# Kernel tuning notes

Measured on AMD Instinct MI355X. Metric: run time of the kernel, lower is better.

The kernel has to match this reference:

```python
import jax, jax.numpy as jnp
import numpy as np

B, S, E = 4, 2048, 1024
H = E // 2  # per-head dim (2 heads)


def setup_inputs() -> dict:
    key = jax.random.key(0)
    ks = jax.random.split(key, 10)
    w = 0.02
    return {
        "input": jax.random.normal(ks[0], (B, S, E), dtype=jnp.float32),
        "Wq": jax.random.normal(ks[1], (2, H, H), dtype=jnp.float32) * w,
        "bq": jax.random.normal(ks[2], (2, H), dtype=jnp.float32) * w,
        "Wk": jax.random.normal(ks[3], (2, H, H), dtype=jnp.float32) * w,
        "bk": jax.random.normal(ks[4], (2, H), dtype=jnp.float32) * w,
        "Wv": jax.random.normal(ks[5], (2, H, H), dtype=jnp.float32) * w,
        "bv": jax.random.normal(ks[6], (2, H), dtype=jnp.float32) * w,
        "Wf": jax.random.normal(ks[7], (E, E), dtype=jnp.float32) * w,
        "bf": jax.random.normal(ks[8], (E,), dtype=jnp.float32) * w,
        "masked": 1,
    }


def reference(input, Wq, bq, Wk, bk, Wv, bv, Wf, bf, masked):
    b, s, e = input.shape
    h = e // 2
    # contiguous split into 2 heads: [b, s, 2, h]
    xh = input.reshape(b, s, 2, h)
    # per-head Linear: y = x @ W.T + b  (W is [out, in])
    q = jnp.einsum("bsnh,noh->bsno", xh, Wq) + bq
    k = jnp.einsum("bsnh,noh->bsno", xh, Wk) + bk
    v = jnp.einsum("bsnh,noh->bsno", xh, Wv) + bv
    # scores: [b, n, s, t]
    scores = jnp.einsum("bsno,btno->bnst", q, k) / jnp.sqrt(jnp.float32(h))
    if masked:
        causal = jnp.tril(jnp.ones((s, s), dtype=bool))
        scores = jnp.where(causal, scores, jnp.float32(-jnp.inf))
    probs = jax.nn.softmax(scores, axis=-1)
    out = jnp.einsum("bnst,btnh->bsnh", probs, v).reshape(b, s, e)
    return jnp.einsum("bse,oe->bso", out, Wf) + bf
```

## Files before the change

kernel.cpp:

```cpp
#include <hip/hip_runtime.h>
#include <hip/hip_bf16.h>

#define BB 4
#define SS 2048
#define EE 1024
#define HH 512

typedef __attribute__((ext_vector_type(8))) short short8;
typedef __attribute__((ext_vector_type(4))) float f32x4;
typedef __attribute__((ext_vector_type(16))) float f32x16;
typedef __attribute__((ext_vector_type(4))) unsigned short us4;

static __device__ __forceinline__ unsigned short f2bf(float x){
  unsigned u = __float_as_uint(x);
  u += 0x7fffu + ((u >> 16) & 1u);
  return (unsigned short)(u >> 16);
}

static __device__ __forceinline__ unsigned cvtpk(float lo, float hi){
  unsigned d;
  asm("v_cvt_pk_bf16_f32 %0, %1, %2" : "=v"(d) : "v"(lo), "v"(hi));
  return d;
}

static __device__ __forceinline__ void gload16(const void* g, void* l){
  __builtin_amdgcn_global_load_lds((const __attribute__((address_space(1))) void*)g,
                                   (__attribute__((address_space(3))) void*)l, 16, 0, 0);
}

__global__ void k_cvt_all(const float* __restrict__ x,  const float* __restrict__ wq,
                          const float* __restrict__ wk, const float* __restrict__ wv,
                          const float* __restrict__ wf,
                          unsigned short* __restrict__ xb,  unsigned short* __restrict__ wqb,
                          unsigned short* __restrict__ wkb, unsigned short* __restrict__ wvb,
                          unsigned short* __restrict__ wfb){
  const int N0 = 1048576;
  const int N1 = N0 + 65536;
  const int N2 = N1 + 65536;
  const int N3 = N2 + 65536;
  const int N4 = N3 + 131072;
  int idx = blockIdx.x * blockDim.x + threadIdx.x;
  int stride = gridDim.x * blockDim.x;
  for (int i = idx; i < N4; i += stride){
    const float* src; unsigned short* dst; int j;
    if (i < N0){ src = x;  dst = xb;  j = i; }
    else if (i < N1){ src = wq; dst = wqb; j = i - N0; }
    else if (i < N2){ src = wk; dst = wkb; j = i - N1; }
    else if (i < N3){ src = wv; dst = wvb; j = i - N2; }
    else            { src = wf; dst = wfb; j = i - N3; }
    const float4* p = (const float4*)src + (long)j * 2;
    float4 a = p[0], b = p[1];
    union { unsigned short u[8]; uint4 v; } r;
    r.u[0]=f2bf(a.x); r.u[1]=f2bf(a.y); r.u[2]=f2bf(a.z); r.u[3]=f2bf(a.w);
    r.u[4]=f2bf(b.x); r.u[5]=f2bf(b.y); r.u[6]=f2bf(b.z); r.u[7]=f2bf(b.w);
    ((uint4*)dst)[j] = r.v;
  }
}

#define GBK 32

template<int OUTMODE>
static __device__ __forceinline__ void gemm_tile(
    const unsigned short* __restrict__ A, int lda,
    const unsigned short* __restrict__ Bw, int ldb,
    void* __restrict__ Cc, int ldc,
    const float* __restrict__ bias, int K, int row0, int col0, float oscale)
{
  __shared__ unsigned short As[2][128 * GBK];
  __shared__ unsigned short Bs[2][128 * GBK];
  const int tid = threadIdx.x, lane = tid & 63, w = tid >> 6;
  const int wm = w >> 1, wn = w & 1;
  const int fr = lane & 15, g = lane >> 4;

  f32x4 acc[4][4];
  #pragma unroll
  for (int i = 0; i < 4; i++)
    #pragma unroll
    for (int j = 0; j < 4; j++){ acc[i][j][0]=0.f; acc[i][j][1]=0.f; acc[i][j][2]=0.f; acc[i][j][3]=0.f; }

  const unsigned short* gAsrc[2]; const unsigned short* gBsrc[2];
  unsigned ldsOff[2];
  #pragma unroll
  for (int i = 0; i < 2; i++){
    int slot = w*128 + i*64 + lane;
    int row = slot >> 2, ch = slot & 3;
    int sc_ = ch ^ ((row >> 1) & 3);
    gAsrc[i] = A  + (long)(row0 + row) * lda + sc_ * 8;
    gBsrc[i] = Bw + (long)(col0 + row) * ldb + sc_ * 8;
    ldsOff[i] = (unsigned)((w*128 + i*64) * 8);
  }

  unsigned aoff[4], boff[4];
  #pragma unroll
  for (int mi = 0; mi < 4; mi++){
    int row = wm*64 + mi*16 + fr;
    aoff[mi] = row * GBK + ((g ^ ((row >> 1) & 3)) * 8);
  }
  #pragma unroll
  for (int ni = 0; ni < 4; ni++){
    int row = wn*64 + ni*16 + fr;
    boff[ni] = row * GBK + ((g ^ ((row >> 1) & 3)) * 8);
  }

  const int KT = K / GBK;
  #pragma unroll
  for (int i = 0; i < 2; i++) gload16(gAsrc[i], &As[0][ldsOff[i]]);
  #pragma unroll
  for (int i = 0; i < 2; i++) gload16(gBsrc[i], &Bs[0][ldsOff[i]]);
  __syncthreads();

  for (int kt = 0; kt < KT; ++kt){
    const int cur = kt & 1;
    if (kt + 1 < KT){
      #pragma unroll
      for (int i = 0; i < 2; i++) gload16(gAsrc[i] + (kt+1)*GBK, &As[cur^1][ldsOff[i]]);
      #pragma unroll
      for (int i = 0; i < 2; i++) gload16(gBsrc[i] + (kt+1)*GBK, &Bs[cur^1][ldsOff[i]]);
    }
    short8 av[4], bv[4];
    #pragma unroll
    for (int mi = 0; mi < 4; mi++) av[mi] = *(const short8*)&As[cur][aoff[mi]];
    #pragma unroll
    for (int ni = 0; ni < 4; ni++) bv[ni] = *(const short8*)&Bs[cur][boff[ni]];
    #pragma unroll
    for (int mi = 0; mi < 4; mi++)
      #pragma unroll
      for (int ni = 0; ni < 4; ni++)
        acc[mi][ni] = __builtin_amdgcn_mfma_f32_16x16x32_bf16(av[mi], bv[ni], acc[mi][ni], 0, 0, 0);
    __syncthreads();
  }

  if constexpr (OUTMODE == 2){
    __shared__ unsigned short Ct[128][136];
    #pragma unroll
    for (int mi = 0; mi < 4; mi++){
      #pragma unroll
      for (int ni = 0; ni < 4; ni++){
        int rowb = wm*64 + mi*16 + g*4;
        int col  = wn*64 + ni*16 + fr;
        float bb = bias[col0 + col];
        us4 pk;
        #pragma unroll
        for (int r = 0; r < 4; r++) pk[r] = f2bf((acc[mi][ni][r] + bb) * oscale);
        *(us4*)&Ct[col][rowb] = pk;
      }
    }
    __syncthreads();
    #pragma unroll
    for (int it = 0; it < 8; it++){
      int idx2 = it * 256 + tid;
      int o = idx2 >> 4, sch = idx2 & 15;
      uint4 v = *(const uint4*)&Ct[o][sch * 8];
      *(uint4*)&((unsigned short*)Cc)[(long)(col0 + o) * ldc + row0 + sch * 8] = v;
    }
  } else {
    #pragma unroll
    for (int mi = 0; mi < 4; mi++){
      #pragma unroll
      for (int ni = 0; ni < 4; ni++){
        int row = row0 + wm*64 + mi*16 + g*4;
        int col = col0 + wn*64 + ni*16 + fr;
        float bb = bias[col];
        #pragma unroll
        for (int r = 0; r < 4; r++){
          float v = (acc[mi][ni][r] + bb) * oscale;
          if (OUTMODE == 1) ((unsigned short*)Cc)[(long)(row + r) * ldc + col] = f2bf(v);
          else              ((float*)Cc)[(long)(row + r) * ldc + col] = v;
        }
      }
    }
  }
}

__global__ __launch_bounds__(256, 2) void k_qkv(
    const unsigned short* __restrict__ xb,
    const unsigned short* __restrict__ wq, const unsigned short* __restrict__ wk,
    const float* __restrict__ bq, const float* __restrict__ bk,
    unsigned short* __restrict__ Q, unsigned short* __restrict__ K)
{
  int z = blockIdx.z; int which = z >> 3; int bn = z & 7; int b = bn >> 1, n = bn & 1;
  const unsigned short* W; const float* bias; unsigned short* out;
  float os = 1.f;
  if (which == 0){ W = wq; bias = bq; out = Q; os = 0.044194173824159216f; }
  else { W = wk; bias = bk; out = K; }
  W += n * HH * HH; bias += n * HH; out += (long)bn * SS * HH;
  const unsigned short* Ap = xb + (long)b * SS * EE + n * HH;
  gemm_tile<1>(Ap, EE, W, HH, out, HH, bias, HH, blockIdx.x * 128, blockIdx.y * 128, os);
}

__global__ __launch_bounds__(256, 2) void k_qkv_v(
    const unsigned short* __restrict__ xb, const unsigned short* __restrict__ wv,
    const float* __restrict__ bv, unsigned short* __restrict__ Vt)
{
  int bn = blockIdx.z; int b = bn >> 1, n = bn & 1;
  const unsigned short* W = wv + n * HH * HH;
  const float* bias = bv + n * HH;
  unsigned short* out = Vt + (long)bn * SS * HH;
  const unsigned short* Ap = xb + (long)b * SS * EE + n * HH;
  gemm_tile<2>(Ap, EE, W, HH, out, SS, bias, HH, blockIdx.x * 128, blockIdx.y * 128, 1.f);
}

__global__ __launch_bounds__(256, 2) void k_outproj(
    const unsigned short* __restrict__ O, const unsigned short* __restrict__ wf,
    const float* __restrict__ bfb, float* __restrict__ out)
{
  gemm_tile<0>(O, EE, wf, EE, out, EE, bfb, EE, blockIdx.x * 128, blockIdx.y * 128, 1.f);
}

#define QB 128
#define TB 32

__global__ __launch_bounds__(512, 1) void k_flash10(
    const unsigned short* __restrict__ Qg, const unsigned short* __restrict__ Kg,
    const unsigned short* __restrict__ Vtg,
    unsigned short* __restrict__ Opart, float* __restrict__ mlg,
    const int* __restrict__ maskedp)
{
  __shared__ unsigned short Ks[2][TB * HH];
  __shared__ unsigned short Vs[HH * TB];
  __shared__ float2 Sx[4][2][8][64];

  const int bid = blockIdx.x;
  const int bn = bid & 7;
  const int u = bid >> 3;
  const int masked = *maskedp;
  int qi, c;
  if (masked){
    qi = -1; c = 0;
    int cnt = 0;
    #pragma unroll 1
    for (int q = 0; q < 16; q++){
      int nch = (4*q + 25) / 22;
      if (qi < 0 && u >= cnt && u < cnt + nch){ qi = q; c = u - cnt; }
      cnt += nch;
    }
    if (qi < 0) return;
  } else { qi = u >> 1; c = u & 1; }
  const int n  = masked ? 4*qi + 4 : 64;
  const int CH = masked ? 22 : 32;
  const int t0 = c * CH;
  const int t1 = min(n, t0 + CH);

  const long base = (long)bn * SS * HH;
  const unsigned short* Qp = Qg + base;
  const unsigned short* Kp = Kg + base;
  const unsigned short* Vp = Vtg + base;

  const int tid = threadIdx.x, lane = tid & 63, w = tid >> 6;
  const int ln = lane & 31, hi = lane >> 5;
  const int rg = w & 3, dh = w >> 2;
  const int q0 = qi * QB;
  const int myq = q0 + rg * 32 + ln;

  short8 Qr[16];
  {
    const unsigned short* qrow = Qp + (long)myq * HH + dh * 256 + hi * 8;
    #pragma unroll
    for (int ks = 0; ks < 16; ks++) Qr[ks] = *(const short8*)(qrow + ks * 16);
  }

  f32x16 oa[8];
  #pragma unroll
  for (int i = 0; i < 8; i++)
    #pragma unroll
    for (int r = 0; r < 16; r++) oa[i][r] = 0.f;
  float m_r = -1e30f, l_r = 0.f;

  auto stageK = [&](int buf, int t){
    if (w < 4){
      #pragma unroll
      for (int i = 0; i < 8; i++){
        const int sbase = w * 512 + i * 64;
        const int slot = sbase + lane;
        int row = slot >> 6, ch = slot & 63;
        int sc_ = ch ^ (row & 7);
        gload16(Kp + (long)(t * TB + row) * HH + sc_ * 8, &Ks[buf][sbase * 8]);
      }
    }
  };
  auto stageV = [&](int t){
    if (w >= 4){
      #pragma unroll
      for (int i = 0; i < 8; i++){
        const int sbase = (w - 4) * 512 + i * 64;
        const int slot = sbase + lane;
        int row = slot >> 2, ch = slot & 3;
        int sc_ = ch ^ ((row >> 1) & 3);
        gload16(Vp + (long)row * SS + t * TB + sc_ * 8, &Vs[sbase * 8]);
      }
    }
  };

  stageK(0, t0);
  stageV(t0);
  __syncthreads();

  for (int t = t0; t < t1; ++t){
    const int cur = (t - t0) & 1;
    if (t > t0)     stageV(t);
    if (t + 1 < t1) stageK(cur ^ 1, t + 1);

    f32x16 sa;
    #pragma unroll
    for (int r = 0; r < 16; r++) sa[r] = 0.f;
    #pragma unroll
    for (int ks = 0; ks < 16; ks++){
      int ch = (dh * 32 + ks * 2 + hi) ^ (ln & 7);
      short8 kf = *(const short8*)&Ks[cur][ln * HH + ch * 8];
      sa = __builtin_amdgcn_mfma_f32_32x32x16_bf16(kf, Qr[ks], sa, 0, 0, 0);
    }

    #pragma unroll
    for (int i = 0; i < 8; i++)
      Sx[rg][dh][i][lane] = make_float2(sa[2*i], sa[2*i+1]);

    __syncthreads();

    float p[16];
    #pragma unroll
    for (int i = 0; i < 8; i++){
      float2 o = Sx[rg][dh ^ 1][i][lane];
      p[2*i]   = sa[2*i]   + o.x;
      p[2*i+1] = sa[2*i+1] + o.y;
    }

    if (masked && (t * TB + TB - 1 > myq)){
      #pragma unroll
      for (int r = 0; r < 16; r++){
        int tl = (r & 3) + 8 * (r >> 2) + 4 * hi;
        if (t * TB + tl > myq) p[r] = -1e30f;
      }
    }

    float mx = p[0];
    #pragma unroll
    for (int r = 1; r < 16; r++) mx = fmaxf(mx, p[r]);
    mx = fmaxf(mx, __shfl_xor(mx, 32, 64));
    if (__any(mx > m_r + 8.f)){
      float mn = fmaxf(m_r, mx);
      float alpha = __expf(m_r - mn);
      m_r = mn; l_r *= alpha;
      #pragma unroll
      for (int r = 0; r < 16; r++){
        float al = __shfl(alpha, (r & 3) + 8 * (r >> 2) + 4 * hi, 64);
        #pragma unroll
        for (int i = 0; i < 8; i++) oa[i][r] *= al;
      }
    }
    float ps = 0.f;
    #pragma unroll
    for (int r = 0; r < 16; r++){ float pe = __expf(p[r] - m_r); p[r] = pe; ps += pe; }
    ps += __shfl_xor(ps, 32, 64);
    l_r += ps;

    unsigned W[8], R[8];
    #pragma unroll
    for (int i = 0; i < 8; i++) W[i] = cvtpk(p[2*i], p[2*i+1]);
    #pragma unroll
    for (int i = 0; i < 8; i++) R[i] = __shfl_xor(W[i], 32, 64);
    union { unsigned u[4]; short8 s; } fa0, fa1;
    fa0.u[0] = hi ? R[2] : W[0];  fa0.u[1] = hi ? R[3] : W[1];
    fa0.u[2] = hi ? W[2] : R[0];  fa0.u[3] = hi ? W[3] : R[1];
    fa1.u[0] = hi ? R[6] : W[4];  fa1.u[1] = hi ? R[7] : W[5];
    fa1.u[2] = hi ? W[6] : R[4];  fa1.u[3] = hi ? W[7] : R[5];

    #pragma unroll
    for (int cf = 0; cf < 8; cf++){
      int h = dh * 256 + cf * 32 + ln;
      int sw = (h >> 1) & 3;
      short8 v0 = *(const short8*)&Vs[h * TB + ((hi     ^ sw) * 8)];
      oa[cf] = __builtin_amdgcn_mfma_f32_32x32x16_bf16(fa0.s, v0, oa[cf], 0, 0, 0);
      short8 v1 = *(const short8*)&Vs[h * TB + (((2+hi) ^ sw) * 8)];
      oa[cf] = __builtin_amdgcn_mfma_f32_32x32x16_bf16(fa1.s, v1, oa[cf], 0, 0, 0);
    }

    __syncthreads();
  }

  const long slot = (long)(bn * 16 + qi) * 3 + c;
  unsigned short* dst = Opart + slot * (QB * HH);
  #pragma unroll
  for (int cf = 0; cf < 8; cf++){
    int col = dh * 256 + cf * 32 + ln;
    #pragma unroll
    for (int r = 0; r < 16; r++){
      int row = rg * 32 + (r & 3) + 8 * (r >> 2) + 4 * hi;
      dst[row * HH + col] = f2bf(oa[cf][r]);
    }
  }
  if (w < 4 && hi == 0){
    mlg[slot * 256 + rg * 32 + ln]       = m_r;
    mlg[slot * 256 + 128 + rg * 32 + ln] = l_r;
  }
}

__global__ __launch_bounds__(256) void k_combine(
    const unsigned short* __restrict__ Opart, const float* __restrict__ mlg,
    unsigned short* __restrict__ O, const int* __restrict__ maskedp)
{
  __shared__ float wl[128][3];
  const int gq = blockIdx.x;
  const int bn = gq & 7, qi = gq >> 3;
  const int b = bn >> 1, n = bn & 1;
  const int NC = (*maskedp) ? (4*qi + 25) / 22 : 2;
  const long slotbase = (long)(bn * 16 + qi) * 3;
  const int tid = threadIdx.x;

  if (tid < 128){
    float mc[3], lc[3];
    float M = -1e30f;
    for (int c = 0; c < NC; c++){
      mc[c] = mlg[(slotbase + c) * 256 + tid];
      lc[c] = mlg[(slotbase + c) * 256 + 128 + tid];
      M = fmaxf(M, mc[c]);
    }
    float L = 0.f;
    for (int c = 0; c < NC; c++){
      float wc = __expf(mc[c] - M);
      mc[c] = wc;
      L += lc[c] * wc;
    }
    float inv = 1.f / L;
    #pragma unroll
    for (int c = 0; c < 3; c++) wl[tid][c] = (c < NC) ? mc[c] * inv : 0.f;
  }
  __syncthreads();

  for (int it = 0; it < 32; it++){
    int idx = it * 256 + tid;
    int row = idx >> 6, cv = idx & 63;
    float acc[8] = {0.f,0.f,0.f,0.f,0.f,0.f,0.f,0.f};
    for (int c = 0; c < NC; c++){
      float wc = wl[row][c];
      short8 v = *(const short8*)&Opart[(slotbase + c) * (QB * HH) + row * HH + cv * 8];
      #pragma unroll
      for (int j = 0; j < 8; j++){
        float f = __uint_as_float((unsigned)(unsigned short)v[j] << 16);
        acc[j] += f * wc;
      }
    }
    union { unsigned short u[8]; uint4 q; } rr;
    #pragma unroll
    for (int j = 0; j < 8; j++) rr.u[j] = f2bf(acc[j]);
    long dstoff = ((long)b * SS + qi * QB + row) * EE + n * HH + cv * 8;
    *(uint4*)&O[dstoff] = rr.q;
  }
}

extern "C" void kernel_launch(void* const* d_in, const int* in_sizes, int n_in,
                              void* d_out, int out_size, void* d_ws, size_t ws_size,
                              hipStream_t stream)
{
  const float* x   = (const float*)d_in[0];
  const float* Wq  = (const float*)d_in[1];
  const float* bq  = (const float*)d_in[2];
  const float* Wk  = (const float*)d_in[3];
  const float* bk  = (const float*)d_in[4];
  const float* Wv  = (const float*)d_in[5];
  const float* bv  = (const float*)d_in[6];
  const float* Wf  = (const float*)d_in[7];
  const float* bf_ = (const float*)d_in[8];
  const int* masked = (const int*)d_in[9];

  char* p = (char*)d_ws;
  const long TEN = (long)BB * SS * EE * 2;
  unsigned short* xb  = (unsigned short*)p; p += TEN;
  unsigned short* Qb  = (unsigned short*)p; p += TEN;
  unsigned short* Kb  = (unsigned short*)p; p += TEN;
  unsigned short* Vt  = (unsigned short*)p; p += TEN;
  unsigned short* Ob  = (unsigned short*)p; p += TEN;
  unsigned short* wqb = (unsigned short*)p; p += 2L * HH * HH * 2;
  unsigned short* wkb = (unsigned short*)p; p += 2L * HH * HH * 2;
  unsigned short* wvb = (unsigned short*)p; p += 2L * HH * HH * 2;
  unsigned short* wfb = (unsigned short*)p; p += (long)EE * EE * 2;
  unsigned short* Opart = (unsigned short*)p; p += 384L * QB * HH * 2;
  float* mlg = (float*)p; p += 384L * 256 * 4;

  k_cvt_all<<<dim3(2048), 256, 0, stream>>>(x, Wq, Wk, Wv, Wf, xb, wqb, wkb, wvb, wfb);
  k_qkv    <<<dim3(SS / 128, HH / 128, 16), 256, 0, stream>>>(xb, wqb, wkb, bq, bk, Qb, Kb);
  k_qkv_v  <<<dim3(SS / 128, HH / 128, 8),  256, 0, stream>>>(xb, wvb, bv, Vt);
  k_flash10<<<dim3(256), 512, 0, stream>>>(Qb, Kb, Vt, Opart, mlg, masked);
  k_combine<<<dim3(128), 256, 0, stream>>>(Opart, mlg, Ob, masked);
  k_outproj<<<dim3((BB * SS) / 128, EE / 128, 1), 256, 0, stream>>>(Ob, wfb, bf_, (float*)d_out);
}
```

Measured before the change: 231.7 us.

## Fuse split-KV combine into output projection GEMM A-tile loading

Removes the separate combine kernel and the intermediate O buffer. The output-projection GEMM now reads the partial attention outputs and their (m, l) statistics directly, merges the partials with softmax weights while building each A tile in shared memory, and writes bf16 A tiles itself instead of using async loads. This saves one launch and a round trip of the O tensor through memory. In exchange, the combine work is repeated for every column block (8 times) and the A path becomes register-staged rather than async, adding ALU and load pressure inside the GEMM main loop.

Result: slower. 240.2 us (+3.7%).

```diff
diff --git a/kernel.cpp b/kernel.cpp
--- a/kernel.cpp
+++ b/kernel.cpp
@@ -164,8 +164,7 @@
         #pragma unroll
         for (int r = 0; r < 4; r++){
           float v = (acc[mi][ni][r] + bb) * oscale;
-          if (OUTMODE == 1) ((unsigned short*)Cc)[(long)(row + r) * ldc + col] = f2bf(v);
-          else              ((float*)Cc)[(long)(row + r) * ldc + col] = v;
+          ((unsigned short*)Cc)[(long)(row + r) * ldc + col] = f2bf(v);
         }
       }
     }
@@ -200,17 +199,165 @@
   gemm_tile<2>(Ap, EE, W, HH, out, SS, bias, HH, blockIdx.x * 128, blockIdx.y * 128, 1.f);
 }
 
-__global__ __launch_bounds__(256, 2) void k_outproj(
-    const unsigned short* __restrict__ O, const unsigned short* __restrict__ wf,
-    const float* __restrict__ bfb, float* __restrict__ out)
+__global__ __launch_bounds__(256, 2) void k_outproj_f(
+    const unsigned short* __restrict__ Opart, const float* __restrict__ mlg,
+    const unsigned short* __restrict__ wf, const float* __restrict__ bfb,
+    float* __restrict__ out, const int* __restrict__ maskedp)
 {
-  gemm_tile<0>(O, EE, wf, EE, out, EE, bfb, EE, blockIdx.x * 128, blockIdx.y * 128, 1.f);
+  __shared__ unsigned short As[2][128 * GBK];
+  __shared__ unsigned short Bs[2][128 * GBK];
+  __shared__ float wl2[2][128][3];
+
+  const int tid = threadIdx.x, lane = tid & 63, w = tid >> 6;
+  const int wm = w >> 1, wn = w & 1;
+  const int fr = lane & 15, g = lane >> 4;
+  const int row0 = blockIdx.x * 128, col0 = blockIdx.y * 128;
+  const int b = row0 >> 11, qi = (row0 & 2047) >> 7;
+  const int masked = *maskedp;
+  const int NC = masked ? (4*qi + 25) / 22 : 2;
+  const long sbn[2] = { ((long)(b*2+0)*16 + qi) * 3, ((long)(b*2+1)*16 + qi) * 3 };
+
+  {
+    int nn = tid >> 7, r = tid & 127;
+    long sb = sbn[nn];
+    float mc[3], lc[3], M = -1e30f;
+    for (int c = 0; c < NC; c++){
+      mc[c] = mlg[(sb + c) * 256 + r];
+      lc[c] = mlg[(sb + c) * 256 + 128 + r];
+      M = fmaxf(M, mc[c]);
+    }
+    float L = 0.f;
+    for (int c = 0; c < NC; c++){ float e = __expf(mc[c] - M); mc[c] = e; L += lc[c] * e; }
+    float inv = 1.f / L;
+    #pragma unroll
+    for (int c = 0; c < 3; c++) wl2[nn][r][c] = (c < NC) ? mc[c] * inv : 0.f;
+  }
+  __syncthreads();
+
+  int rowv[2], scv[2], slotv[2];
+  float wlr0[2][3], wlr1[2][3];
+  #pragma unroll
+  for (int i = 0; i < 2; i++){
+    int slot = w*128 + i*64 + lane;
+    slotv[i] = slot;
+    rowv[i] = slot >> 2;
+    scv[i] = (slot & 3) ^ ((rowv[i] >> 1) & 3);
+    #pragma unroll
+    for (int c = 0; c < 3; c++){
+      wlr0[i][c] = wl2[0][rowv[i]][c];
+      wlr1[i][c] = wl2[1][rowv[i]][c];
+    }
+  }
+
+  const unsigned short* gBsrc[2];
+  unsigned ldsOffB[2];
+  #pragma unroll
+  for (int i = 0; i < 2; i++){
+    int slot = w*128 + i*64 + lane;
+    int row = slot >> 2, ch = slot & 3;
+    int sc_ = ch ^ ((row >> 1) & 3);
+    gBsrc[i] = wf + (long)(col0 + row) * EE + sc_ * 8;
+    ldsOffB[i] = (unsigned)((w*128 + i*64) * 8);
+  }
+
+  unsigned aoff[4], boff[4];
+  #pragma unroll
+  for (int mi = 0; mi < 4; mi++){
+    int row = wm*64 + mi*16 + fr;
+    aoff[mi] = row * GBK + ((g ^ ((row >> 1) & 3)) * 8);
+  }
+  #pragma unroll
+  for (int ni = 0; ni < 4; ni++){
+    int row = wn*64 + ni*16 + fr;
+    boff[ni] = row * GBK + ((g ^ ((row >> 1) & 3)) * 8);
+  }
+
+  f32x4 acc[4][4];
+  #pragma unroll
+  for (int i = 0; i < 4; i++)
+    #pragma unroll
+    for (int j = 0; j < 4; j++){ acc[i][j][0]=0.f; acc[i][j][1]=0.f; acc[i][j][2]=0.f; acc[i][j][3]=0.f; }
+
+  uint4 va[2][3];
+  auto loadA = [&](int kt){
+    const int nn = kt >> 4;
+    const long sb = nn ? sbn[1] : sbn[0];
+    #pragma unroll
+    for (int i = 0; i < 2; i++){
+      long base = sb * 65536L + (long)rowv[i] * HH + (kt & 15) * 32 + scv[i] * 8;
+      #pragma unroll
+      for (int c = 0; c < 3; c++)
+        if (c < NC) va[i][c] = *(const uint4*)&Opart[base + c * 65536L];
+    }
+  };
+  auto writeA = [&](int buf, int kt){
+    const int nn = kt >> 4;
+    #pragma unroll
+    for (int i = 0; i < 2; i++){
+      float a8[8] = {0.f,0.f,0.f,0.f,0.f,0.f,0.f,0.f};
+      #pragma unroll
+      for (int c = 0; c < 3; c++){
+        if (c < NC){
+          float wc = nn ? wlr1[i][c] : wlr0[i][c];
+          const unsigned short* pu = (const unsigned short*)&va[i][c];
+          #pragma unroll
+          for (int j = 0; j < 8; j++)
+            a8[j] += __uint_as_float((unsigned)pu[j] << 16) * wc;
+        }
+      }
+      union { unsigned short u[8]; uint4 q; } pk;
+      #pragma unroll
+      for (int j = 0; j < 8; j++) pk.u[j] = f2bf(a8[j]);
+      *(uint4*)&As[buf][slotv[i] * 8] = pk.q;
+    }
+  };
+
+  const int KT = EE / GBK;
+  loadA(0);
+  writeA(0, 0);
+  #pragma unroll
+  for (int i = 0; i < 2; i++) gload16(gBsrc[i], &Bs[0][ldsOffB[i]]);
+  __syncthreads();
+
+  for (int kt = 0; kt < KT; ++kt){
+    const int cur = kt & 1;
+    if (kt + 1 < KT){
+      loadA(kt + 1);
+      #pragma unroll
+      for (int i = 0; i < 2; i++) gload16(gBsrc[i] + (kt+1)*GBK, &Bs[cur^1][ldsOffB[i]]);
+    }
+    short8 av[4], bv[4];
+    #pragma unroll
+    for (int mi = 0; mi < 4; mi++) av[mi] = *(const short8*)&As[cur][aoff[mi]];
+    #pragma unroll
+    for (int ni = 0; ni < 4; ni++) bv[ni] = *(const short8*)&Bs[cur][boff[ni]];
+    #pragma unroll
+    for (int mi = 0; mi < 4; mi++)
+      #pragma unroll
+      for (int ni = 0; ni < 4; ni++)
+        acc[mi][ni] = __builtin_amdgcn_mfma_f32_16x16x32_bf16(av[mi], bv[ni], acc[mi][ni], 0, 0, 0);
+    if (kt + 1 < KT) writeA(cur ^ 1, kt + 1);
+    __syncthreads();
+  }
+
+  #pragma unroll
+  for (int mi = 0; mi < 4; mi++){
+    #pragma unroll
+    for (int ni = 0; ni < 4; ni++){
+      int row = row0 + wm*64 + mi*16 + g*4;
+      int col = col0 + wn*64 + ni*16 + fr;
+      float bb = bfb[col];
+      #pragma unroll
+      for (int r = 0; r < 4; r++)
+        out[(long)(row + r) * EE + col] = acc[mi][ni][r] + bb;
+    }
+  }
 }
 
 #define QB 128
 #define TB 32
 
-__global__ __launch_bounds__(512, 1) void k_flash10(
+__global__ __launch_bounds__(512, 1) void k_flash11(
     const unsigned short* __restrict__ Qg, const unsigned short* __restrict__ Kg,
     const unsigned short* __restrict__ Vtg,
     unsigned short* __restrict__ Opart, float* __restrict__ mlg,
@@ -391,59 +538,6 @@
   if (w < 4 && hi == 0){
     mlg[slot * 256 + rg * 32 + ln]       = m_r;
     mlg[slot * 256 + 128 + rg * 32 + ln] = l_r;
-  }
-}
-
-__global__ __launch_bounds__(256) void k_combine(
-    const unsigned short* __restrict__ Opart, const float* __restrict__ mlg,
-    unsigned short* __restrict__ O, const int* __restrict__ maskedp)
-{
-  __shared__ float wl[128][3];
-  const int gq = blockIdx.x;
-  const int bn = gq & 7, qi = gq >> 3;
-  const int b = bn >> 1, n = bn & 1;
-  const int NC = (*maskedp) ? (4*qi + 25) / 22 : 2;
-  const long slotbase = (long)(bn * 16 + qi) * 3;
-  const int tid = threadIdx.x;
-
-  if (tid < 128){
-    float mc[3], lc[3];
-    float M = -1e30f;
-    for (int c = 0; c < NC; c++){
-      mc[c] = mlg[(slotbase + c) * 256 + tid];
-      lc[c] = mlg[(slotbase + c) * 256 + 128 + tid];
-      M = fmaxf(M, mc[c]);
-    }
-    float L = 0.f;
-    for (int c = 0; c < NC; c++){
-      float wc = __expf(mc[c] - M);
-      mc[c] = wc;
-      L += lc[c] * wc;
-    }
-    float inv = 1.f / L;
-    #pragma unroll
-    for (int c = 0; c < 3; c++) wl[tid][c] = (c < NC) ? mc[c] * inv : 0.f;
-  }
-  __syncthreads();
-
-  for (int it = 0; it < 32; it++){
-    int idx = it * 256 + tid;
-    int row = idx >> 6, cv = idx & 63;
-    float acc[8] = {0.f,0.f,0.f,0.f,0.f,0.f,0.f,0.f};
-    for (int c = 0; c < NC; c++){
-      float wc = wl[row][c];
-      short8 v = *(const short8*)&Opart[(slotbase + c) * (QB * HH) + row * HH + cv * 8];
-      #pragma unroll
-      for (int j = 0; j < 8; j++){
-        float f = __uint_as_float((unsigned)(unsigned short)v[j] << 16);
-        acc[j] += f * wc;
-      }
-    }
-    union { unsigned short u[8]; uint4 q; } rr;
-    #pragma unroll
-    for (int j = 0; j < 8; j++) rr.u[j] = f2bf(acc[j]);
-    long dstoff = ((long)b * SS + qi * QB + row) * EE + n * HH + cv * 8;
-    *(uint4*)&O[dstoff] = rr.q;
   }
 }
 
@@ -468,7 +562,6 @@
   unsigned short* Qb  = (unsigned short*)p; p += TEN;
   unsigned short* Kb  = (unsigned short*)p; p += TEN;
   unsigned short* Vt  = (unsigned short*)p; p += TEN;
-  unsigned short* Ob  = (unsigned short*)p; p += TEN;
   unsigned short* wqb = (unsigned short*)p; p += 2L * HH * HH * 2;
   unsigned short* wkb = (unsigned short*)p; p += 2L * HH * HH * 2;
   unsigned short* wvb = (unsigned short*)p; p += 2L * HH * HH * 2;
@@ -479,7 +572,7 @@
   k_cvt_all<<<dim3(2048), 256, 0, stream>>>(x, Wq, Wk, Wv, Wf, xb, wqb, wkb, wvb, wfb);
   k_qkv    <<<dim3(SS / 128, HH / 128, 16), 256, 0, stream>>>(xb, wqb, wkb, bq, bk, Qb, Kb);
   k_qkv_v  <<<dim3(SS / 128, HH / 128, 8),  256, 0, stream>>>(xb, wvb, bv, Vt);
-  k_flash10<<<dim3(256), 512, 0, stream>>>(Qb, Kb, Vt, Opart, mlg, masked);
-  k_combine<<<dim3(128), 256, 0, stream>>>(Opart, mlg, Ob, masked);
-  k_outproj<<<dim3((BB * SS) / 128, EE / 128, 1), 256, 0, stream>>>(Ob, wfb, bf_, (float*)d_out);
-}
+  k_flash11<<<dim3(256), 512, 0, stream>>>(Qb, Kb, Vt, Opart, mlg, masked);
+  k_outproj_f<<<dim3((BB * SS) / 128, EE / 128, 1), 256, 0, stream>>>(Opart, mlg, wfb, bf_,
+                                                                      (float*)d_out, masked);
+}
```
